# Kernel optimization log

Measured on AMD Instinct MI355X. Metric: run time of the kernel, lower is better.

## Reference

```python
import jax, jax.numpy as jnp
import numpy as np

B, S, D, H, I, E, K, L, C = 4, 1024, 512, 8, 2048, 8, 2, 4, 4
D2 = D // 2
EPS = 1e-5  # torch LayerNorm default


def _ln(x, w, b):
    m = jnp.mean(x, -1, keepdims=True)
    v = jnp.mean((x - m) ** 2, -1, keepdims=True)
    return (x - m) * jax.lax.rsqrt(v + EPS) * w + b


def setup_inputs() -> dict:
    key = jax.random.key(0)
    ks = iter(jax.random.split(key, 40))
    n = lambda shp, s=0.02: jax.random.normal(next(ks), shp, dtype=jnp.float32) * s
    return {
        'embeddings': jax.random.normal(next(ks), (B, S, D), jnp.float32),
        'attention_mask': jnp.ones((B, S), jnp.float32),
        'in_w': n((L, 3 * D, D)), 'in_b': jnp.zeros((L, 3 * D)),
        'out_w': n((L, D, D)), 'out_b': jnp.zeros((L, D)),
        'ln1_w': jnp.ones((L, D)), 'ln1_b': jnp.zeros((L, D)),
        'ln2_w': jnp.ones((L, D)), 'ln2_b': jnp.zeros((L, D)),
        'gate_w': n((L, E, D)),
        'e_w1': n((L, E, D, I)), 'e_b1': jnp.zeros((L, E, I)),
        'e_w2': n((L, E, I, D)), 'e_b2': jnp.zeros((L, E, D)),
        'mln_w': jnp.ones((L, D)), 'mln_b': jnp.zeros((L, D)),
        'fln_w': jnp.ones((D,)), 'fln_b': jnp.zeros((D,)),
        'pool_w': n((D, D)), 'pool_b': jnp.zeros((D,)),
        'cls_w': n((C, D)), 'cls_b': jnp.zeros((C,)),
        'cf_w1': n((D2, D)), 'cf_b1': jnp.zeros((D2,)),
        'cf_w2': n((1, D2)), 'cf_b2': jnp.zeros((1,)),
    }


def _forward(embeddings, attention_mask, in_w, in_b, out_w, out_b, ln1_w, ln1_b,
             ln2_w, ln2_b, gate_w, e_w1, e_b1, e_w2, e_b2, mln_w, mln_b,
             fln_w, fln_b, pool_w, pool_b, cls_w, cls_b, cf_w1, cf_b1, cf_w2, cf_b2):
    x = embeddings
    dh = D // H
    total_aux = jnp.float32(0.0)
    for l in range(L):
        # --- self-attention (eval mode, dropout off) ---
        h = _ln(x, ln1_w[l], ln1_b[l])
        qkv = h @ in_w[l].T + in_b[l]                       # (B,S,3D)
        q, k, v = jnp.split(qkv, 3, axis=-1)
        q = q.reshape(B, S, H, dh).transpose(0, 2, 1, 3)
        k = k.reshape(B, S, H, dh).transpose(0, 2, 1, 3)
        v = v.reshape(B, S, H, dh).transpose(0, 2, 1, 3)
        scores = jnp.einsum('bhqd,bhkd->bhqk', q, k) / (dh ** 0.5)
        attn = jax.nn.softmax(scores, axis=-1)
        ctx = jnp.einsum('bhqk,bhkd->bhqd', attn, v).transpose(0, 2, 1, 3).reshape(B, S, D)
        x = x + (ctx @ out_w[l].T + out_b[l])
        # --- MoE FFN (residual is the post-norm2 tensor, per source) ---
        h = _ln(x, ln2_w[l], ln2_b[l])
        flat = h.reshape(-1, D)                             # (T,D)
        probs = jax.nn.softmax(flat @ gate_w[l].T, axis=-1) # (T,E)
        vals, idx = jax.lax.top_k(probs, K)                 # (T,K)
        vals = vals / vals.sum(-1, keepdims=True)
        onehot = jax.nn.one_hot(idx, E, dtype=flat.dtype)   # (T,K,E)
        comb = jnp.einsum('tk,tke->te', vals, onehot)       # (T,E) per-expert weight, 0 if not selected
        mid = jax.nn.gelu(jnp.einsum('td,edf->tef', flat, e_w1[l]) + e_b1[l], approximate=False)
        eout = jnp.einsum('tef,efd->ted', mid, e_w2[l]) + e_b2[l]
        moe_out = jnp.einsum('ted,te->td', eout, comb).reshape(B, S, D)
        moe_out = moe_out * attention_mask[..., None]
        x = _ln(h + moe_out, mln_w[l], mln_b[l])
        usage = onehot.sum((0, 1)) / flat.shape[0]
        total_aux = total_aux + jnp.mean((usage - 1.0 / E) ** 2)
    # --- head ---
    x = _ln(x, fln_w, fln_b)
    me = attention_mask[..., None]
    pooled = (x * me).sum(1) / jnp.maximum(me.sum(1), 1e-9)
    pooled = jnp.tanh(pooled @ pool_w.T + pool_b)
    logits = pooled @ cls_w.T + cls_b
    conf = jax.nn.sigmoid(jax.nn.relu(pooled @ cf_w1.T + cf_b1) @ cf_w2.T + cf_b2)
    return logits, total_aux / L, conf


def reference(embeddings, attention_mask, in_w, in_b, out_w, out_b, ln1_w, ln1_b,
              ln2_w, ln2_b, gate_w, e_w1, e_b1, e_w2, e_b2, mln_w, mln_b,
              fln_w, fln_b, pool_w, pool_b, cls_w, cls_b, cf_w1, cf_b1, cf_w2, cf_b2):
    return _forward(embeddings, attention_mask, in_w, in_b, out_w, out_b, ln1_w, ln1_b,
                    ln2_w, ln2_b, gate_w, e_w1, e_b1, e_w2, e_b2, mln_w, mln_b,
                    fln_w, fln_b, pool_w, pool_b, cls_w, cls_b, cf_w1, cf_b1, cf_w2, cf_b2)
```

## Files before the change

### kernel.cpp

```cpp
#include <hip/hip_runtime.h>
#include <math.h>

#define B_ 4
#define S_ 1024
#define D_ 512
#define H_ 8
#define DH_ 64
#define I_ 2048
#define E_ 8
#define L_ 4
#define T_ 4096

using bf16x8 = __attribute__((ext_vector_type(8))) __bf16;
using f32x4  = __attribute__((ext_vector_type(4))) float;

typedef __attribute__((address_space(1))) const void gvoid;
typedef __attribute__((address_space(3))) void lvoid;
__device__ __forceinline__ void gl_lds16(const void* g, void* l){
  __builtin_amdgcn_global_load_lds((gvoid*)g, (lvoid*)l, 16, 0, 0);
}

__device__ __forceinline__ float wred_sum(float v){
#pragma unroll
  for(int m=32;m>0;m>>=1) v += __shfl_xor(v, m, 64);
  return v;
}
__device__ __forceinline__ unsigned short f2bf(float f){
  unsigned x = __float_as_uint(f);
  unsigned r = (x + 0x7FFFu + ((x>>16)&1u)) >> 16;
  return (unsigned short)r;
}
__device__ __forceinline__ float bf2f(unsigned short u){
  return __uint_as_float(((unsigned)u)<<16);
}
__device__ __forceinline__ unsigned pk2(float a, float b){
  return (unsigned)f2bf(a) | ((unsigned)f2bf(b)<<16);
}

template<int BM, int BN, bool MOE, bool GATHER, bool OUT_BF16, int ACT, bool ADD_IN>
__global__ __launch_bounds__(256)
void gemm_k(const unsigned short* __restrict__ A, const unsigned short* __restrict__ Bv,
            void* Cp, const float* __restrict__ bias, const float* addin,
            int M, int N, int K, int lda, int ldb, int ldc,
            int hdiv, long sAb, long sAh, long sBb, long sBh, long sCb, long sCh,
            float scale,
            const int* __restrict__ moff, const int* __restrict__ mcnt,
            const int* __restrict__ rowtok, const int* __restrict__ btab,
            long sBe, int biasStride, int nby)
{
  constexpr int BK = 64;
  constexpr int WM = BM/2, WN = BN/2, FM = WM/16, FNN = WN/16;
  constexpr int RPC = 2048/BK;
  constexpr int NA = BM/RPC, NB = BN/RPC;
  constexpr int NLD = NA + NB;
  __shared__ unsigned short As[2*BM*BK];
  __shared__ unsigned short Bs[2*BN*BK];

  const int tid = threadIdx.x, wid = tid>>6, lane = tid&63;
  const int wy = wid>>1, wx = wid&1, ln16 = lane&15, q8 = (lane>>4)*8;

  const int nwg = gridDim.x, cpx = nwg >> 3;
  const int lin = blockIdx.x;
  const int wg  = (lin & 7)*cpx + (lin >> 3);
  const int bxi = wg / nby, byi = wg % nby;

  int m0 = bxi*BM;
  const int n0 = byi*BN;

  float* Cf = nullptr; unsigned short* Ch = nullptr;
  const float* biasp = bias;
  const unsigned short* Bp = Bv;
  int seg = 0, cnt = M;

  if constexpr (MOE){
    int tv = btab[bxi];
    if (tv < 0) return;
    int e = tv>>8;
    m0 = (tv&255)*BM;
    seg = moff[e]; cnt = mcnt[e];
    Bp = Bv + (long)e*sBe;
    if constexpr (OUT_BF16) Ch = (unsigned short*)Cp; else Cf = (float*)Cp;
    if (biasp) biasp += (long)e*biasStride;
  } else {
    int z = blockIdx.z, zb = z/hdiv, zh = z%hdiv;
    A  += (long)zb*sAb + (long)zh*sAh;
    Bp += (long)zb*sBb + (long)zh*sBh;
    long coff = (long)zb*sCb + (long)zh*sCh;
    if constexpr (OUT_BF16) Ch = (unsigned short*)Cp + coff; else Cf = ((float*)Cp) + coff;
    if constexpr (ADD_IN) addin += coff;
  }

  const int srow = tid >> 3;
  const int scol = (tid & 7) * 8;
  long ga[NA], gb[NB];
#pragma unroll
  for (int j=0; j<NA; j++){
    int r = m0 + j*RPC + srow;
    if constexpr (MOE){
      r = min(r, cnt-1);
      long gr = GATHER ? (long)rowtok[seg+r] : (long)(seg+r);
      ga[j] = gr*lda + scol;
    } else {
      ga[j] = (long)min(r, M-1)*lda + scol;
    }
  }
#pragma unroll
  for (int j=0; j<NB; j++){
    int bn = min(n0 + j*RPC + srow, N-1);
    gb[j] = (long)bn*ldb + scol;
  }

  f32x4 acc[FM][FNN];
#pragma unroll
  for(int i=0;i<FM;i++)
#pragma unroll
    for(int j=0;j<FNN;j++){ f32x4 z = {0.f,0.f,0.f,0.f}; acc[i][j] = z; }

  const int nt = K/BK;
  int cur = 0;
#pragma unroll
  for (int j=0; j<NA; j++) gl_lds16(A + ga[j], As + j*2048 + wid*512);
#pragma unroll
  for (int j=0; j<NB; j++) gl_lds16(Bp + gb[j], Bs + j*2048 + wid*512);

  for (int t = 0; t < nt; ++t){
    const int cb = cur;
    if (t+1 < nt){
      const int nb2 = cur^1;
      const int k0 = (t+1)*BK;
#pragma unroll
      for (int j=0; j<NA; j++) gl_lds16(A + ga[j] + k0, As + nb2*BM*BK + j*2048 + wid*512);
#pragma unroll
      for (int j=0; j<NB; j++) gl_lds16(Bp + gb[j] + k0, Bs + nb2*BN*BK + j*2048 + wid*512);
      asm volatile("s_waitcnt vmcnt(%0)" :: "n"(NLD) : "memory");
    } else {
      asm volatile("s_waitcnt vmcnt(0)" ::: "memory");
    }
    __builtin_amdgcn_s_barrier();
    __builtin_amdgcn_sched_barrier(0);
#pragma unroll
    for (int kk=0; kk<2; kk++){
      bf16x8 fa[FM], fb[FNN];
#pragma unroll
      for(int i=0;i<FM;i++) fa[i] = *(const bf16x8*)&As[cb*BM*BK + (wy*WM + i*16 + ln16)*BK + kk*32 + q8];
#pragma unroll
      for(int j=0;j<FNN;j++) fb[j] = *(const bf16x8*)&Bs[cb*BN*BK + (wx*WN + j*16 + ln16)*BK + kk*32 + q8];
#pragma unroll
      for(int i=0;i<FM;i++)
#pragma unroll
        for(int j=0;j<FNN;j++)
          acc[i][j] = __builtin_amdgcn_mfma_f32_16x16x32_bf16(fa[i], fb[j], acc[i][j], 0, 0, 0);
    }
    __builtin_amdgcn_sched_barrier(0);
    __builtin_amdgcn_s_barrier();
    cur ^= 1;
  }

#pragma unroll
  for(int i=0;i<FM;i++){
    int mbase = m0 + wy*WM + i*16 + (lane>>4)*4;
#pragma unroll
    for(int j=0;j<FNN;j++){
      int n = n0 + wx*WN + j*16 + ln16;
      float bv = biasp ? biasp[n] : 0.f;
      f32x4 v = acc[i][j];
#pragma unroll
      for(int r=0;r<4;r++){
        int m = mbase + r;
        if (m < cnt){
          float x = v[r]*scale + bv;
          if constexpr (ACT == 1) x = 0.5f*x*(1.f + erff(x*0.70710678118654752f));
          long ci = (long)(MOE ? seg + m : m)*ldc + n;
          if constexpr (ADD_IN) x += addin[ci];
          if constexpr (OUT_BF16) Ch[ci] = f2bf(x);
          else Cf[ci] = x;
        }
      }
    }
  }
}

__global__ __launch_bounds__(256)
void flash_k(const unsigned short* __restrict__ qkvb, const unsigned short* __restrict__ Vt,
             unsigned short* __restrict__ ctx)
{
  __shared__ unsigned short Pl[4][16*72];
  const int qt = blockIdx.x, z = blockIdx.y, b = z>>3, h = z&7;
  const int wid = threadIdx.x>>6, lane = threadIdx.x&63;
  const int ln16 = lane&15, g = lane>>4;
  const int q0 = qt*64 + wid*16;
  unsigned short* Pw = &Pl[wid][0];

  const unsigned short* Qp = qkvb + (long)(b*1024 + q0 + ln16)*1536 + h*64 + g*8;
  bf16x8 qf0 = *(const bf16x8*)Qp;
  bf16x8 qf1 = *(const bf16x8*)(Qp + 32);
  const unsigned short* Kbase = qkvb + (long)b*1024*1536 + 512 + h*64 + g*8;
  const unsigned short* Vbase = Vt + (long)z*65536 + g*8;

  float m_s[4], l_s[4];
  f32x4 oacc[4];
#pragma unroll
  for(int r=0;r<4;r++){ m_s[r] = -1e30f; l_s[r] = 0.f; }
#pragma unroll
  for(int j=0;j<4;j++){ f32x4 zz = {0.f,0.f,0.f,0.f}; oacc[j] = zz; }

  for (int t = 0; t < 16; ++t){
    bf16x8 kf[4][2], vf[4][2];
#pragma unroll
    for(int j=0;j<4;j++){
      const unsigned short* kp = Kbase + (long)(t*64 + j*16 + ln16)*1536;
      kf[j][0] = *(const bf16x8*)kp;
      kf[j][1] = *(const bf16x8*)(kp + 32);
      const unsigned short* vp = Vbase + (long)(j*16 + ln16)*1024 + t*64;
      vf[j][0] = *(const bf16x8*)vp;
      vf[j][1] = *(const bf16x8*)(vp + 32);
    }
    f32x4 sacc[4];
#pragma unroll
    for(int j=0;j<4;j++){ f32x4 zz = {0.f,0.f,0.f,0.f}; sacc[j] = zz; }
#pragma unroll
    for(int j=0;j<4;j++){
      sacc[j] = __builtin_amdgcn_mfma_f32_16x16x32_bf16(qf0, kf[j][0], sacc[j], 0,0,0);
      sacc[j] = __builtin_amdgcn_mfma_f32_16x16x32_bf16(qf1, kf[j][1], sacc[j], 0,0,0);
    }
#pragma unroll
    for(int j=0;j<4;j++)
#pragma unroll
      for(int r=0;r<4;r++) sacc[j][r] *= 0.125f;
    float alpha[4];
#pragma unroll
    for(int r=0;r<4;r++){
      float mx = fmaxf(fmaxf(sacc[0][r], sacc[1][r]), fmaxf(sacc[2][r], sacc[3][r]));
#pragma unroll
      for(int m=1;m<16;m<<=1) mx = fmaxf(mx, __shfl_xor(mx, m, 64));
      float mn = fmaxf(m_s[r], mx);
      alpha[r] = __expf(m_s[r] - mn);
      m_s[r] = mn;
    }
#pragma unroll
    for(int j=0;j<4;j++)
#pragma unroll
      for(int r=0;r<4;r++) sacc[j][r] = __expf(sacc[j][r] - m_s[r]);
#pragma unroll
    for(int r=0;r<4;r++){
      float rs = sacc[0][r]+sacc[1][r]+sacc[2][r]+sacc[3][r];
#pragma unroll
      for(int m=1;m<16;m<<=1) rs += __shfl_xor(rs, m, 64);
      l_s[r] = l_s[r]*alpha[r] + rs;
    }
#pragma unroll
    for(int j=0;j<4;j++)
#pragma unroll
      for(int r=0;r<4;r++) oacc[j][r] *= alpha[r];
#pragma unroll
    for(int j=0;j<4;j++)
#pragma unroll
      for(int r=0;r<4;r++)
        Pw[(g*4+r)*72 + j*16 + ln16] = f2bf(sacc[j][r]);
    bf16x8 pf0 = *(const bf16x8*)&Pw[ln16*72 + g*8];
    bf16x8 pf1 = *(const bf16x8*)&Pw[ln16*72 + 32 + g*8];
#pragma unroll
    for(int j=0;j<4;j++){
      oacc[j] = __builtin_amdgcn_mfma_f32_16x16x32_bf16(pf0, vf[j][0], oacc[j], 0,0,0);
      oacc[j] = __builtin_amdgcn_mfma_f32_16x16x32_bf16(pf1, vf[j][1], oacc[j], 0,0,0);
    }
  }
#pragma unroll
  for(int r=0;r<4;r++){
    float inv = 1.f/l_s[r];
    long row = (long)(b*1024 + q0 + g*4 + r)*512 + h*64;
#pragma unroll
    for(int j=0;j<4;j++)
      ctx[row + j*16 + ln16] = f2bf(oacc[j][r]*inv);
  }
}

template<bool OUT_BF16>
__global__ __launch_bounds__(256)
void ln_w_k(const float* __restrict__ in, const float* __restrict__ w,
            const float* __restrict__ bb, void* __restrict__ outp)
{
  int row = blockIdx.x*4 + (threadIdx.x>>6), lane = threadIdx.x&63;
  const float4* p = (const float4*)(in + (long)row*512 + lane*8);
  float4 a = p[0], c = p[1];
  float s = a.x+a.y+a.z+a.w + c.x+c.y+c.z+c.w;
  float q = a.x*a.x+a.y*a.y+a.z*a.z+a.w*a.w + c.x*c.x+c.y*c.y+c.z*c.z+c.w*c.w;
  s = wred_sum(s); q = wred_sum(q);
  float mean = s*(1.f/512.f);
  float var  = q*(1.f/512.f) - mean*mean;
  float inv  = rsqrtf(var + 1e-5f);
  const float4* wp = (const float4*)(w + lane*8);
  const float4* bp = (const float4*)(bb + lane*8);
  float4 w0 = wp[0], w1 = wp[1], b0 = bp[0], b1 = bp[1];
  float o0 = (a.x-mean)*inv*w0.x + b0.x, o1 = (a.y-mean)*inv*w0.y + b0.y;
  float o2 = (a.z-mean)*inv*w0.z + b0.z, o3 = (a.w-mean)*inv*w0.w + b0.w;
  float o4 = (c.x-mean)*inv*w1.x + b1.x, o5 = (c.y-mean)*inv*w1.y + b1.y;
  float o6 = (c.z-mean)*inv*w1.z + b1.z, o7 = (c.w-mean)*inv*w1.w + b1.w;
  if constexpr (OUT_BF16){
    *(uint4*)((unsigned short*)outp + (long)row*512 + lane*8) =
      make_uint4(pk2(o0,o1), pk2(o2,o3), pk2(o4,o5), pk2(o6,o7));
  } else {
    float4* op = (float4*)((float*)outp + (long)row*512 + lane*8);
    op[0] = make_float4(o0,o1,o2,o3);
    op[1] = make_float4(o4,o5,o6,o7);
  }
}

__global__ __launch_bounds__(256)
void ln2route_k(const float* __restrict__ in, const float* __restrict__ w,
                const float* __restrict__ bb, unsigned short* __restrict__ h2,
                const float* __restrict__ gw,
                int* __restrict__ tok_e, float* __restrict__ tok_w)
{
  int tok = blockIdx.x*4 + (threadIdx.x>>6), lane = threadIdx.x&63;
  const float4* p = (const float4*)(in + (long)tok*512 + lane*8);
  float4 a = p[0], c = p[1];
  float s = a.x+a.y+a.z+a.w + c.x+c.y+c.z+c.w;
  float q = a.x*a.x+a.y*a.y+a.z*a.z+a.w*a.w + c.x*c.x+c.y*c.y+c.z*c.z+c.w*c.w;
  s = wred_sum(s); q = wred_sum(q);
  float mean = s*(1.f/512.f);
  float var  = q*(1.f/512.f) - mean*mean;
  float inv  = rsqrtf(var + 1e-5f);
  const float4* wp = (const float4*)(w + lane*8);
  const float4* bp = (const float4*)(bb + lane*8);
  float4 w0 = wp[0], w1 = wp[1], b0 = bp[0], b1 = bp[1];
  float o[8];
  o[0] = (a.x-mean)*inv*w0.x + b0.x; o[1] = (a.y-mean)*inv*w0.y + b0.y;
  o[2] = (a.z-mean)*inv*w0.z + b0.z; o[3] = (a.w-mean)*inv*w0.w + b0.w;
  o[4] = (c.x-mean)*inv*w1.x + b1.x; o[5] = (c.y-mean)*inv*w1.y + b1.y;
  o[6] = (c.z-mean)*inv*w1.z + b1.z; o[7] = (c.w-mean)*inv*w1.w + b1.w;
  *(uint4*)(h2 + (long)tok*512 + lane*8) =
    make_uint4(pk2(o[0],o[1]), pk2(o[2],o[3]), pk2(o[4],o[5]), pk2(o[6],o[7]));
  float lg[8];
#pragma unroll
  for(int e=0;e<8;e++){
    const float4* gr = (const float4*)(gw + e*512 + lane*8);
    float4 g0 = gr[0], g1 = gr[1];
    float d = o[0]*g0.x + o[1]*g0.y + o[2]*g0.z + o[3]*g0.w
            + o[4]*g1.x + o[5]*g1.y + o[6]*g1.z + o[7]*g1.w;
    lg[e] = wred_sum(d);
  }
  if (lane == 0){
    float mx = lg[0];
#pragma unroll
    for(int e=1;e<8;e++) mx = fmaxf(mx, lg[e]);
    float pr[8];
#pragma unroll
    for(int e=0;e<8;e++) pr[e] = expf(lg[e]-mx);
    int e0 = 0; float p0 = pr[0];
#pragma unroll
    for(int e=1;e<8;e++) if (pr[e] > p0){ p0 = pr[e]; e0 = e; }
    int e1 = -1; float p1 = -1.f;
#pragma unroll
    for(int e=0;e<8;e++) if (e != e0 && pr[e] > p1){ p1 = pr[e]; e1 = e; }
    float invp = 1.f/(p0+p1);
    tok_e[2*tok] = e0; tok_e[2*tok+1] = e1;
    tok_w[2*tok] = p0*invp; tok_w[2*tok+1] = p1*invp;
  }
}

__global__ __launch_bounds__(1024)
void plan_scatter_k(const int* __restrict__ tok_e, const float* __restrict__ tok_w,
                    int* __restrict__ offs, int* __restrict__ cnts, float* __restrict__ aux,
                    int* __restrict__ btab, int* __restrict__ btab64,
                    int* __restrict__ rowtok, float* __restrict__ roww, int* __restrict__ rowof)
{
  __shared__ int hist[8];
  __shared__ int offsS[8];
  __shared__ int base[8];
  const int t = threadIdx.x;
  if (t < 8) hist[t] = 0;
  __syncthreads();
  int e[8]; float w[8];
#pragma unroll
  for (int i=0;i<8;i++){
    e[i] = tok_e[t + i*1024];
    w[i] = tok_w[t + i*1024];
    atomicAdd(&hist[e[i]], 1);
  }
  __syncthreads();
  if (t == 0){
    int o = 0, idx = 0, idx2 = 0; float a = 0.f;
    for (int ee=0; ee<8; ee++){
      offsS[ee] = o;
      int c = hist[ee];
      o += c;
      float u = (float)c*(1.f/4096.f) - 0.125f;
      a += u*u;
      int nb = (c + 127) >> 7;
      for (int j=0;j<nb;j++) btab[idx++] = (ee<<8)|j;
      int nb2 = (c + 63) >> 6;
      for (int j=0;j<nb2;j++) btab64[idx2++] = (ee<<8)|j;
    }
    while (idx < 80) btab[idx++] = -1;
    while (idx2 < 144) btab64[idx2++] = -1;
    *aux += a*(1.f/8.f);
  }
  __syncthreads();
  if (t < 8){
    cnts[t] = hist[t];
    offs[t] = offsS[t];
    base[t] = offsS[t];
  }
  __syncthreads();
#pragma unroll
  for (int i=0;i<8;i++){
    int pos = atomicAdd(&base[e[i]], 1);
    int gi = t + i*1024;
    rowtok[pos] = gi>>1;
    roww[pos] = w[i];
    rowof[gi] = pos;
  }
}

__global__ __launch_bounds__(256)
void ln_moe_k(const float* __restrict__ eout, const int* __restrict__ rowof,
              const float* __restrict__ roww, const float* __restrict__ mask,
              const unsigned short* __restrict__ h2,
              const float* __restrict__ w, const float* __restrict__ bb,
              float* __restrict__ outp)
{
  int tok = blockIdx.x*4 + (threadIdx.x>>6), lane = threadIdx.x&63;
  int r0 = rowof[2*tok], r1 = rowof[2*tok+1];
  float w0w = roww[r0], w1w = roww[r1], mk = mask[tok];
  const float4* ap = (const float4*)(eout + (long)r0*512 + lane*8);
  const float4* bp2 = (const float4*)(eout + (long)r1*512 + lane*8);
  float4 a0 = ap[0], a1 = ap[1], c0 = bp2[0], c1 = bp2[1];
  uint4 hu = *(const uint4*)(h2 + (long)tok*512 + lane*8);
  const unsigned short* hh = (const unsigned short*)&hu;
  float v[8];
  v[0] = bf2f(hh[0]) + (a0.x*w0w + c0.x*w1w)*mk;
  v[1] = bf2f(hh[1]) + (a0.y*w0w + c0.y*w1w)*mk;
  v[2] = bf2f(hh[2]) + (a0.z*w0w + c0.z*w1w)*mk;
  v[3] = bf2f(hh[3]) + (a0.w*w0w + c0.w*w1w)*mk;
  v[4] = bf2f(hh[4]) + (a1.x*w0w + c1.x*w1w)*mk;
  v[5] = bf2f(hh[5]) + (a1.y*w0w + c1.y*w1w)*mk;
  v[6] = bf2f(hh[6]) + (a1.z*w0w + c1.z*w1w)*mk;
  v[7] = bf2f(hh[7]) + (a1.w*w0w + c1.w*w1w)*mk;
  float s = 0.f, q = 0.f;
#pragma unroll
  for(int i=0;i<8;i++){ s += v[i]; q += v[i]*v[i]; }
  s = wred_sum(s); q = wred_sum(q);
  float mean = s*(1.f/512.f);
  float var  = q*(1.f/512.f) - mean*mean;
  float inv  = rsqrtf(var + 1e-5f);
  const float4* wp = (const float4*)(w + lane*8);
  const float4* bpp = (const float4*)(bb + lane*8);
  float4 w0 = wp[0], w1 = wp[1], b0 = bpp[0], b1 = bpp[1];
  float wv[8] = {w0.x,w0.y,w0.z,w0.w,w1.x,w1.y,w1.z,w1.w};
  float bv[8] = {b0.x,b0.y,b0.z,b0.w,b1.x,b1.y,b1.z,b1.w};
  float4* op = (float4*)(outp + (long)tok*512 + lane*8);
  op[0] = make_float4((v[0]-mean)*inv*wv[0]+bv[0], (v[1]-mean)*inv*wv[1]+bv[1],
                      (v[2]-mean)*inv*wv[2]+bv[2], (v[3]-mean)*inv*wv[3]+bv[3]);
  op[1] = make_float4((v[4]-mean)*inv*wv[4]+bv[4], (v[5]-mean)*inv*wv[5]+bv[5],
                      (v[6]-mean)*inv*wv[6]+bv[6], (v[7]-mean)*inv*wv[7]+bv[7]);
}

__global__ __launch_bounds__(256)
void vt_k(const unsigned short* __restrict__ qkvb, unsigned short* __restrict__ Vt)
{
  __shared__ unsigned short tile[64][80];
  int z = blockIdx.y, b = z>>3, h = z&7;
  int t = threadIdx.x;
  int kk = t>>2, dd = (t&3)*16;
  int dd2 = t>>2, kk2 = (t&3)*16;
  for (int c = 0; c < 4; ++c){
    int k0 = (blockIdx.x*4 + c)*64;
    const unsigned short* p = qkvb + ((long)(b*1024 + k0 + kk))*1536 + 1024 + h*64 + dd;
    uint4 u0 = *(const uint4*)p, u1 = *(const uint4*)(p+8);
    __syncthreads();
    *(uint4*)&tile[kk][dd] = u0;
    *(uint4*)&tile[kk][dd+8] = u1;
    __syncthreads();
    uint4 o0, o1;
    unsigned short* s0 = (unsigned short*)&o0;
    unsigned short* s1 = (unsigned short*)&o1;
#pragma unroll
    for(int j=0;j<8;j++){ s0[j] = tile[kk2+j][dd2]; s1[j] = tile[kk2+8+j][dd2]; }
    unsigned short* o = Vt + (long)z*65536 + (long)dd2*1024 + k0 + kk2;
    *(uint4*)o = o0; *(uint4*)(o+8) = o1;
  }
}

__global__ __launch_bounds__(256)
void transpose_cast_k(const float* __restrict__ in, unsigned short* __restrict__ outp,
                      int R, int C, int ZL)
{
  __shared__ float tile[64][65];
  int t = threadIdx.x;
  int rr = t>>2, cc = (t&3)*16;
  int cc2 = t>>2, rr2 = (t&3)*16;
  int c0 = blockIdx.x*64, r0 = blockIdx.y*64;
  for (int zi = 0; zi < ZL; ++zi){
    long zoff = (long)(blockIdx.z*ZL + zi) * R * C;
    const float* pin = in + zoff + (long)(r0+rr)*C + c0 + cc;
    float4 v0=*(const float4*)pin, v1=*(const float4*)(pin+4), v2=*(const float4*)(pin+8), v3=*(const float4*)(pin+12);
    __syncthreads();
    tile[rr][cc+0]=v0.x; tile[rr][cc+1]=v0.y; tile[rr][cc+2]=v0.z; tile[rr][cc+3]=v0.w;
    tile[rr][cc+4]=v1.x; tile[rr][cc+5]=v1.y; tile[rr][cc+6]=v1.z; tile[rr][cc+7]=v1.w;
    tile[rr][cc+8]=v2.x; tile[rr][cc+9]=v2.y; tile[rr][cc+10]=v2.z; tile[rr][cc+11]=v2.w;
    tile[rr][cc+12]=v3.x; tile[rr][cc+13]=v3.y; tile[rr][cc+14]=v3.z; tile[rr][cc+15]=v3.w;
    __syncthreads();
    unsigned tmp[8];
#pragma unroll
    for(int jj=0;jj<8;jj++)
      tmp[jj] = pk2(tile[rr2+2*jj][cc2], tile[rr2+2*jj+1][cc2]);
    uint4* dst = (uint4*)(outp + zoff + (long)(c0+cc2)*R + r0 + rr2);
    dst[0] = make_uint4(tmp[0],tmp[1],tmp[2],tmp[3]);
    dst[1] = make_uint4(tmp[4],tmp[5],tmp[6],tmp[7]);
  }
}

__global__ __launch_bounds__(256)
void cast_bf16_k(const float* __restrict__ in, unsigned short* __restrict__ outp, int n8)
{
  for (int i = blockIdx.x*256 + threadIdx.x; i < n8; i += gridDim.x*256){
    const float4* p = (const float4*)(in + (long)i*8);
    float4 a = p[0], b = p[1];
    *(uint4*)(outp + (long)i*8) = make_uint4(pk2(a.x,a.y), pk2(a.z,a.w), pk2(b.x,b.y), pk2(b.z,b.w));
  }
}

__global__ __launch_bounds__(256)
void pool2_k(const float* __restrict__ h, const float* __restrict__ mask, float* __restrict__ pooled)
{
  int b = blockIdx.x, sc = blockIdx.y, t = threadIdx.x;
  float a0 = 0.f, a1 = 0.f;
  const float* mb = mask + b*1024 + sc*128;
  const float* hbase = h + ((long)b*1024 + sc*128)*512;
  for (int s = 0; s < 128; ++s){
    float mk = mb[s];
    const float* r = hbase + (long)s*512;
    a0 += r[t]*mk; a1 += r[t+256]*mk;
  }
  pooled[((b*8 + sc)*512) + t] = a0;
  pooled[((b*8 + sc)*512) + t + 256] = a1;
}

__global__ __launch_bounds__(256)
void head_final_k(const float* __restrict__ pooled, const float* __restrict__ mask,
                  const float* __restrict__ pool_w, const float* __restrict__ pool_b,
                  const float* __restrict__ cls_w, const float* __restrict__ cls_b,
                  const float* __restrict__ cf_w1, const float* __restrict__ cf_b1,
                  const float* __restrict__ cf_w2, const float* __restrict__ cf_b2,
                  const float* __restrict__ aux, float* __restrict__ out)
{
  int b = blockIdx.x, t = threadIdx.x, wid = t>>6, lane = t&63;
  __shared__ __align__(16) float pld[512];
  __shared__ __align__(16) float p2[512];
  __shared__ float red[4];
  float ds = 0.f;
  for(int s=t; s<1024; s+=256) ds += mask[b*1024 + s];
  ds = wred_sum(ds);
  if (lane==0) red[wid] = ds;
  __syncthreads();
  float denom = fmaxf(red[0]+red[1]+red[2]+red[3], 1e-9f);
  float s0 = 0.f, s1 = 0.f;
#pragma unroll
  for(int sc=0;sc<8;sc++){
    s0 += pooled[((b*8+sc)*512) + t];
    s1 += pooled[((b*8+sc)*512) + t + 256];
  }
  pld[t]     = s0/denom;
  pld[t+256] = s1/denom;
  __syncthreads();
#pragma unroll
  for(int jj=0;jj<2;jj++){
    int j = t + jj*256;
    const float4* wr = (const float4*)(pool_w + (long)j*512);
    float acc = 0.f;
    for(int i=0;i<128;i++){
      float4 w4 = wr[i]; float4 x4 = ((const float4*)pld)[i];
      acc += w4.x*x4.x + w4.y*x4.y + w4.z*x4.z + w4.w*x4.w;
    }
    p2[j] = tanhf(acc + pool_b[j]);
  }
  __syncthreads();
  if (t < 4){
    const float4* wr = (const float4*)(cls_w + (long)t*512);
    float acc = 0.f;
    for(int i=0;i<128;i++){
      float4 w4 = wr[i]; float4 x4 = ((const float4*)p2)[i];
      acc += w4.x*x4.x + w4.y*x4.y + w4.z*x4.z + w4.w*x4.w;
    }
    out[b*4 + t] = acc + cls_b[t];
  }
  {
    const float4* wr = (const float4*)(cf_w1 + (long)t*512);
    float acc = 0.f;
    for(int i=0;i<128;i++){
      float4 w4 = wr[i]; float4 x4 = ((const float4*)p2)[i];
      acc += w4.x*x4.x + w4.y*x4.y + w4.z*x4.z + w4.w*x4.w;
    }
    acc = fmaxf(acc + cf_b1[t], 0.f) * cf_w2[t];
    acc = wred_sum(acc);
    __syncthreads();
    if (lane==0) red[wid] = acc;
    __syncthreads();
    if (t == 0){
      float sum = red[0]+red[1]+red[2]+red[3];
      out[17 + b] = 1.f/(1.f + expf(-(sum + cf_b2[0])));
    }
  }
  if (b == 0 && t == 0) out[16] = aux[0]*0.25f;
}

extern "C" void kernel_launch(void* const* d_in, const int* in_sizes, int n_in,
                              void* d_out, int out_size, void* d_ws, size_t ws_size,
                              hipStream_t stream)
{
  (void)in_sizes; (void)n_in; (void)out_size;
  const float* emb    = (const float*)d_in[0];
  const float* mask   = (const float*)d_in[1];
  const float* in_w   = (const float*)d_in[2];
  const float* in_b   = (const float*)d_in[3];
  const float* out_w  = (const float*)d_in[4];
  const float* out_b  = (const float*)d_in[5];
  const float* ln1_w  = (const float*)d_in[6];
  const float* ln1_b  = (const float*)d_in[7];
  const float* ln2_w  = (const float*)d_in[8];
  const float* ln2_b  = (const float*)d_in[9];
  const float* gate_w = (const float*)d_in[10];
  const float* e_w1   = (const float*)d_in[11];
  const float* e_b1   = (const float*)d_in[12];
  const float* e_w2   = (const float*)d_in[13];
  const float* e_b2   = (const float*)d_in[14];
  const float* mln_w  = (const float*)d_in[15];
  const float* mln_b  = (const float*)d_in[16];
  const float* fln_w  = (const float*)d_in[17];
  const float* fln_b  = (const float*)d_in[18];
  const float* pool_w = (const float*)d_in[19];
  const float* pool_b = (const float*)d_in[20];
  const float* cls_w  = (const float*)d_in[21];
  const float* cls_b  = (const float*)d_in[22];
  const float* cf_w1  = (const float*)d_in[23];
  const float* cf_b1  = (const float*)d_in[24];
  const float* cf_w2  = (const float*)d_in[25];
  const float* cf_b2  = (const float*)d_in[26];
  float* out = (float*)d_out;
  char* ws = (char*)d_ws;

  const size_t MiB = 1024*1024;
  if (ws_size < 218*MiB) return;

  float*          x     = (float*)(ws + 0*MiB);
  unsigned short* hb    = (unsigned short*)(ws + 8*MiB);
  unsigned short* qkvb  = (unsigned short*)(ws + 12*MiB);
  unsigned short* ctx   = (unsigned short*)(ws + 24*MiB);
  unsigned short* Vt    = (unsigned short*)(ws + 28*MiB);
  unsigned short* mid   = (unsigned short*)(ws + 32*MiB);
  float*          eout  = (float*)(ws + 64*MiB);
  float*          fout  = (float*)(ws + 64*MiB);
  unsigned short* w1t   = (unsigned short*)(ws + 80*MiB);
  unsigned short* w2t   = (unsigned short*)(ws + 144*MiB);
  unsigned short* inwb  = (unsigned short*)(ws + 208*MiB);
  unsigned short* outwb = (unsigned short*)(ws + 214*MiB);
  char* misc = ws + 216*MiB;
  int*   counts  = (int*)(misc + 0);
  int*   offs    = (int*)(misc + 64);
  float* aux     = (float*)(misc + 128);
  int*   btab    = (int*)(misc + 256);
  int*   btab64  = (int*)(misc + 1024);
  float* pooled  = (float*)(misc + 4096);
  int*   tok_e   = (int*)(misc + 81920);
  float* tok_w   = (float*)(misc + 114688);
  int*   rowtok  = (int*)(misc + 147456);
  float* roww    = (float*)(misc + 180224);
  int*   rowof   = (int*)(misc + 212992);

  hipMemcpyAsync(x, emb, (size_t)T_*D_*4, hipMemcpyDeviceToDevice, stream);
  hipMemsetAsync(aux, 0, 4, stream);
  cast_bf16_k<<<512, 256, 0, stream>>>(in_w, inwb, L_*3*D_*D_/8);
  cast_bf16_k<<<256, 256, 0, stream>>>(out_w, outwb, L_*D_*D_/8);
  transpose_cast_k<<<dim3(I_/64, D_/64, 4), 256, 0, stream>>>(e_w1, w1t, D_, I_, 8);
  transpose_cast_k<<<dim3(D_/64, I_/64, 4), 256, 0, stream>>>(e_w2, w2t, I_, D_, 8);

  for (int l=0; l<L_; l++){
    const float* inbl  = in_b  + (size_t)l*3*D_;
    const float* outbl = out_b + (size_t)l*D_;
    const float* gwl   = gate_w + (size_t)l*E_*D_;
    const float* eb1l  = e_b1 + (size_t)l*E_*I_;
    const float* eb2l  = e_b2 + (size_t)l*E_*D_;
    const unsigned short* inwbl  = inwb + (size_t)l*3*D_*D_;
    const unsigned short* outwbl = outwb + (size_t)l*D_*D_;
    const unsigned short* w1tl = w1t + (size_t)l*E_*I_*D_;
    const unsigned short* w2tl = w2t + (size_t)l*E_*D_*I_;

    ln_w_k<true><<<T_/4, 256, 0, stream>>>(x, ln1_w + (size_t)l*D_, ln1_b + (size_t)l*D_, hb);
    gemm_k<64,128,false,false,true,0,false><<<dim3(768,1,1), 256, 0, stream>>>(
      hb, inwbl, qkvb, inbl, nullptr, T_, 3*D_, D_, D_, D_, 3*D_,
      1, 0,0,0,0,0,0, 1.f, nullptr, nullptr, nullptr, nullptr, 0, 0, 12);
    vt_k<<<dim3(4,32), 256, 0, stream>>>(qkvb, Vt);
    flash_k<<<dim3(16,32), 256, 0, stream>>>(qkvb, Vt, ctx);
    gemm_k<64,64,false,false,false,0,true><<<dim3(512,1,1), 256, 0, stream>>>(
      ctx, outwbl, x, outbl, x, T_, D_, D_, D_, D_, D_,
      1, 0,0,0,0,0,0, 1.f, nullptr, nullptr, nullptr, nullptr, 0, 0, 8);
    ln2route_k<<<T_/4, 256, 0, stream>>>(x, ln2_w + (size_t)l*D_, ln2_b + (size_t)l*D_,
                                         hb, gwl, tok_e, tok_w);
    plan_scatter_k<<<1, 1024, 0, stream>>>(tok_e, tok_w, offs, counts, aux, btab, btab64,
                                           rowtok, roww, rowof);
    gemm_k<128,128,true,true,true,1,false><<<dim3(1136,1,1), 256, 0, stream>>>(
      hb, w1tl, mid, eb1l, nullptr, 2*T_, I_, D_, D_, D_, I_,
      1, 0,0,0,0,0,0, 1.f, offs, counts, rowtok, btab, (long)I_*D_, I_, 16);
    gemm_k<64,128,true,false,false,0,false><<<dim3(544,1,1), 256, 0, stream>>>(
      mid, w2tl, eout, eb2l, nullptr, 2*T_, D_, I_, I_, I_, D_,
      1, 0,0,0,0,0,0, 1.f, offs, counts, nullptr, btab64, (long)D_*I_, D_, 4);
    ln_moe_k<<<T_/4, 256, 0, stream>>>(eout, rowof, roww, mask, hb,
                                       mln_w + (size_t)l*D_, mln_b + (size_t)l*D_, x);
  }
  ln_w_k<false><<<T_/4, 256, 0, stream>>>(x, fln_w, fln_b, fout);
  pool2_k<<<dim3(4,8), 256, 0, stream>>>(fout, mask, pooled);
  head_final_k<<<4, 256, 0, stream>>>(pooled, mask, pool_w, pool_b, cls_w, cls_b,
                                      cf_w1, cf_b1, cf_w2, cf_b2, aux, out);
}
```

Measured before the change: 1.490 ms.

## Swizzle GEMM LDS layout and restructure main loop with single barrier

The GEMM kernel now XOR-swizzles the 16-byte column chunks of its LDS tiles, both when writing through global_load_lds and when reading MFMA fragments, to avoid LDS bank conflicts. The main loop drops the trailing barrier and uses one wait-plus-barrier per iteration. Next-tile prefetches for A and B are interleaved between the two MFMA k-halves, and s_setprio is raised around the MFMA bursts. The aim is less LDS conflict stall and better overlap of global loads with math. In exchange, the loop now waits for all outstanding loads each iteration, and the correctness of overwriting the alternate buffer rests on that single barrier.

Result: faster. 1.456 ms (-2.3%).

```diff
diff --git a/kernel.cpp b/kernel.cpp
--- a/kernel.cpp
+++ b/kernel.cpp
@@ -52,12 +52,11 @@
   constexpr int WM = BM/2, WN = BN/2, FM = WM/16, FNN = WN/16;
   constexpr int RPC = 2048/BK;
   constexpr int NA = BM/RPC, NB = BN/RPC;
-  constexpr int NLD = NA + NB;
   __shared__ unsigned short As[2*BM*BK];
   __shared__ unsigned short Bs[2*BN*BK];
 
   const int tid = threadIdx.x, wid = tid>>6, lane = tid&63;
-  const int wy = wid>>1, wx = wid&1, ln16 = lane&15, q8 = (lane>>4)*8;
+  const int wy = wid>>1, wx = wid&1, ln16 = lane&15;
 
   const int nwg = gridDim.x, cpx = nwg >> 3;
   const int lin = blockIdx.x;
@@ -91,7 +90,7 @@
   }
 
   const int srow = tid >> 3;
-  const int scol = (tid & 7) * 8;
+  const int scol = ((tid & 7) ^ (srow & 7)) * 8;
   long ga[NA], gb[NB];
 #pragma unroll
   for (int j=0; j<NA; j++){
@@ -117,43 +116,64 @@
     for(int j=0;j<FNN;j++){ f32x4 z = {0.f,0.f,0.f,0.f}; acc[i][j] = z; }
 
   const int nt = K/BK;
-  int cur = 0;
+  const int rsw = ln16 & 7;
+  const int u0 = ((lane>>4)     ^ rsw) * 8;
+  const int u1 = ((4+(lane>>4)) ^ rsw) * 8;
+
 #pragma unroll
   for (int j=0; j<NA; j++) gl_lds16(A + ga[j], As + j*2048 + wid*512);
 #pragma unroll
   for (int j=0; j<NB; j++) gl_lds16(Bp + gb[j], Bs + j*2048 + wid*512);
 
   for (int t = 0; t < nt; ++t){
-    const int cb = cur;
-    if (t+1 < nt){
-      const int nb2 = cur^1;
-      const int k0 = (t+1)*BK;
-#pragma unroll
-      for (int j=0; j<NA; j++) gl_lds16(A + ga[j] + k0, As + nb2*BM*BK + j*2048 + wid*512);
-#pragma unroll
-      for (int j=0; j<NB; j++) gl_lds16(Bp + gb[j] + k0, Bs + nb2*BN*BK + j*2048 + wid*512);
-      asm volatile("s_waitcnt vmcnt(%0)" :: "n"(NLD) : "memory");
-    } else {
-      asm volatile("s_waitcnt vmcnt(0)" ::: "memory");
-    }
+    const int cb = t & 1;
+    const unsigned short* Ab = As + cb*BM*BK;
+    const unsigned short* Bb = Bs + cb*BN*BK;
+    unsigned short* An = As + (cb^1)*BM*BK;
+    unsigned short* Bn = Bs + (cb^1)*BN*BK;
+    const bool pf = (t+1 < nt);
+    const long k0n = (long)(t+1)*BK;
+
+    asm volatile("s_waitcnt vmcnt(0)" ::: "memory");
     __builtin_amdgcn_s_barrier();
     __builtin_amdgcn_sched_barrier(0);
-#pragma unroll
-    for (int kk=0; kk<2; kk++){
+
+    if (pf){
+#pragma unroll
+      for (int j=0; j<NA; j++) gl_lds16(A + ga[j] + k0n, An + j*2048 + wid*512);
+    }
+    {
       bf16x8 fa[FM], fb[FNN];
 #pragma unroll
-      for(int i=0;i<FM;i++) fa[i] = *(const bf16x8*)&As[cb*BM*BK + (wy*WM + i*16 + ln16)*BK + kk*32 + q8];
-#pragma unroll
-      for(int j=0;j<FNN;j++) fb[j] = *(const bf16x8*)&Bs[cb*BN*BK + (wx*WN + j*16 + ln16)*BK + kk*32 + q8];
+      for(int i=0;i<FM;i++) fa[i] = *(const bf16x8*)&Ab[(wy*WM + i*16 + ln16)*BK + u0];
+#pragma unroll
+      for(int j=0;j<FNN;j++) fb[j] = *(const bf16x8*)&Bb[(wx*WN + j*16 + ln16)*BK + u0];
+      __builtin_amdgcn_s_setprio(1);
 #pragma unroll
       for(int i=0;i<FM;i++)
 #pragma unroll
         for(int j=0;j<FNN;j++)
           acc[i][j] = __builtin_amdgcn_mfma_f32_16x16x32_bf16(fa[i], fb[j], acc[i][j], 0, 0, 0);
-    }
-    __builtin_amdgcn_sched_barrier(0);
-    __builtin_amdgcn_s_barrier();
-    cur ^= 1;
+      __builtin_amdgcn_s_setprio(0);
+    }
+    if (pf){
+#pragma unroll
+      for (int j=0; j<NB; j++) gl_lds16(Bp + gb[j] + k0n, Bn + j*2048 + wid*512);
+    }
+    {
+      bf16x8 fa[FM], fb[FNN];
+#pragma unroll
+      for(int i=0;i<FM;i++) fa[i] = *(const bf16x8*)&Ab[(wy*WM + i*16 + ln16)*BK + u1];
+#pragma unroll
+      for(int j=0;j<FNN;j++) fb[j] = *(const bf16x8*)&Bb[(wx*WN + j*16 + ln16)*BK + u1];
+      __builtin_amdgcn_s_setprio(1);
+#pragma unroll
+      for(int i=0;i<FM;i++)
+#pragma unroll
+        for(int j=0;j<FNN;j++)
+          acc[i][j] = __builtin_amdgcn_mfma_f32_16x16x32_bf16(fa[i], fb[j], acc[i][j], 0, 0, 0);
+      __builtin_amdgcn_s_setprio(0);
+    }
   }
 
 #pragma unroll
```
